# Optimization experiments

Measured on AMD Instinct MI355X. Metric: run time of the kernel, lower is better.

Reference implementation:

```python
import jax, jax.numpy as jnp
import numpy as np

B, TD, TC = 64, 800, 80
ENC, H, MA, MO = 128, 400, 10, 20
OUT = MO * 6 + 1  # 121


def _lstm(x, h0, c0, Wih, Whh, bih, bhh):
    # x: (B,T,I); PyTorch gate order i,f,g,o
    xg = jnp.einsum('bti,gi->btg', x, Wih) + (bih + bhh)  # (B,T,4H)
    def step(carry, xg_t):
        h, c = carry
        g = xg_t + h @ Whh.T
        i, f, gg, o = jnp.split(g, 4, axis=-1)
        c = jax.nn.sigmoid(f) * c + jax.nn.sigmoid(i) * jnp.tanh(gg)
        h = jax.nn.sigmoid(o) * jnp.tanh(c)
        return (h, c), h
    (_, _), hs = jax.lax.scan(step, (h0, c0), xg.transpose(1, 0, 2))
    return hs.transpose(1, 0, 2)  # (B,T,H)


def setup_inputs() -> dict:
    key = jax.random.key(0)
    ks = jax.random.split(key, 16)
    s = 0.05
    rn = lambda k, sh, sc=1.0: jax.random.normal(k, sh, jnp.float32) * sc
    I1 = 3 + ENC + H
    return {
        'strokes': rn(ks[0], (B, TD, 3)),
        'context': rn(ks[1], (B, TC, ENC)),
        'context_mask': jnp.ones((B, TC), jnp.float32),
        'h_0': rn(ks[2], (3, 2 * H), s),
        'Wih0': rn(ks[3], (4 * H, 3), s), 'Whh0': rn(ks[4], (4 * H, H), s),
        'bih0': jnp.zeros((4 * H,), jnp.float32), 'bhh0': jnp.zeros((4 * H,), jnp.float32),
        'Wih1': rn(ks[5], (4 * H, I1), s), 'Whh1': rn(ks[6], (4 * H, H), s),
        'bih1': jnp.zeros((4 * H,), jnp.float32), 'bhh1': jnp.zeros((4 * H,), jnp.float32),
        'Wih2': rn(ks[7], (4 * H, I1), s), 'Whh2': rn(ks[8], (4 * H, H), s),
        'bih2': jnp.zeros((4 * H,), jnp.float32), 'bhh2': jnp.zeros((4 * H,), jnp.float32),
        'attn_W': rn(ks[9], (3 * MA, H), s), 'attn_b': jnp.zeros((3 * MA,), jnp.float32),
        'out_W': rn(ks[10], (OUT, 3 * H), s), 'out_b': jnp.zeros((OUT,), jnp.float32),
    }


def reference(strokes, context, context_mask, h_0,
              Wih0, Whh0, bih0, bhh0,
              Wih1, Whh1, bih1, bhh1,
              Wih2, Whh2, bih2, bhh2,
              attn_W, attn_b, out_W, out_b):
    bsz = strokes.shape[0]
    # initial states: h_0[l] split into (h, c)
    init = [(jnp.broadcast_to(h_0[l, :H], (bsz, H)), jnp.broadcast_to(h_0[l, H:], (bsz, H))) for l in range(3)]

    h0s = _lstm(strokes, init[0][0], init[0][1], Wih0, Whh0, bih0, bhh0)  # (B,TD,H)

    # Gaussian monotonic attention
    p = jnp.exp(h0s @ attn_W.T + attn_b)  # (B,TD,3MA)
    alpha, beta, kappa = jnp.split(p, 3, axis=-1)
    kappa = jnp.cumsum(0.2 * kappa, axis=1)  # (B,TD,MA)
    u = jnp.arange(TC, dtype=jnp.float32)  # (TC,)
    # phi: (B,TD,TC)
    diff = kappa[:, :, None, :] - u[None, None, :, None]
    phi = jnp.sum(alpha[:, :, None, :] * jnp.exp(-beta[:, :, None, :] * diff * diff), axis=-1)
    w = jnp.einsum('btu,bue->bte', phi * context_mask[:, None, :], context)  # (B,TD,ENC)

    x1 = jnp.concatenate([strokes, h0s, w], axis=2)
    h1s = _lstm(x1, init[1][0], init[1][1], Wih1, Whh1, bih1, bhh1)
    x2 = jnp.concatenate([strokes, h1s, w], axis=2)
    h2s = _lstm(x2, init[2][0], init[2][1], Wih2, Whh2, bih2, bhh2)

    outputs = jnp.concatenate([h0s, h1s, h2s], axis=-1) @ out_W.T + out_b  # (B,TD,121)
    return outputs
```

## Files before the change

kernel.cpp:

```cpp
#include <hip/hip_runtime.h>
#include <stdint.h>

typedef unsigned short u16;
typedef __attribute__((ext_vector_type(8))) short bf16x8;
typedef __attribute__((ext_vector_type(4))) float f32x4;
typedef __attribute__((ext_vector_type(4))) int   i32x4;
typedef __attribute__((ext_vector_type(4))) unsigned short u16x4;

#define DI static __device__ __forceinline__

constexpr int B_   = 64;
constexpr int TD   = 800;
constexpr int TC   = 80;
constexpr int ENC  = 128;
constexpr int H    = 400;
constexpr int OUTN = 121;

constexpr int HP   = 416;
constexpr int KT_H = 13;
constexpr int KOP  = 1216;
constexpr int NOP  = 128;
constexpr int NBL  = 25;
constexpr int NBA  = 32;
constexpr int CSTR = 32;
constexpr int FSLOT= 32;

constexpr size_t HB_B  = (size_t)(TD+1)*B_*HP*2;
constexpr size_t WBF_B = (size_t)TD*B_*ENC*2;
constexpr size_t STR_B = (size_t)TD*B_*4*4;
constexpr size_t APK_B = (size_t)NBL*4*KT_H*64*8*2;
constexpr size_t WF_B  = (size_t)NBL*4*17*64*8*2;
constexpr size_t LOC_B = (size_t)2*B_*HP*2;

constexpr size_t OFF_HB0 = 0;
constexpr size_t OFF_HB1 = OFF_HB0 + HB_B;
constexpr size_t OFF_HB2 = OFF_HB1 + HB_B;
constexpr size_t OFF_HLO = OFF_HB2 + HB_B;
constexpr size_t OFF_WBF = OFF_HLO + HB_B;
constexpr size_t OFF_STR = OFF_WBF + WBF_B;
constexpr size_t OFF_APKH= OFF_STR + STR_B;
constexpr size_t OFF_APKL= OFF_APKH + 3*APK_B;
constexpr size_t OFF_WF1 = OFF_APKL + APK_B;
constexpr size_t OFF_WF2 = OFF_WF1 + WF_B;
constexpr size_t OFF_OUW = OFF_WF2 + WF_B;
constexpr size_t OFF_BIA = OFF_OUW + (size_t)NOP*KOP*2;
constexpr size_t OFF_CNT = OFF_BIA + (size_t)3*1600*4;
constexpr size_t OFF_XCC = OFF_CNT + (size_t)4*FSLOT*CSTR*4;
constexpr size_t OFF_FLG = OFF_XCC + (size_t)3*FSLOT*CSTR*4;
constexpr size_t OFF_HL0 = OFF_FLG + (size_t)3*FSLOT*CSTR*4;
constexpr size_t OFF_LL0 = OFF_HL0 + LOC_B;
constexpr size_t OFF_HL1 = OFF_LL0 + LOC_B;
constexpr size_t OFF_HL2 = OFF_HL1 + LOC_B;
constexpr size_t WS_NEED = OFF_HL2 + LOC_B + 256;

constexpr int LDS_DUMP = 0;
constexpr int LDS_CL   = 66560;
constexpr int LDS_EX   = 70656;
constexpr int LDS_W3   = 140288;
constexpr int LDS_BIAS = 141056;
constexpr int LDS_VERD = 141312;
constexpr int LDSB     = 141568;
constexpr int ALDS_CTX = 0;
constexpr int ALDS_ATW = 81920;
constexpr int ALDS_H   = 130040;
constexpr int ALDS_PHI = 133240;
constexpr int ALDS_MSK = 133880;
constexpr int ALDS_KAP = 134520;
constexpr int ALDS_P   = 134600;
constexpr int ALDS_PPS = 134840;

DI u16 f2b(float f){ union{float f; unsigned u;} v; v.f=f; unsigned r = v.u + 0x7FFFu + ((v.u>>16)&1u); return (u16)(r>>16); }
DI float b2f(u16 h){ union{unsigned u; float f;} v; v.u=((unsigned)h)<<16; return v.f; }
DI float sigm(float x){ return 1.f/(1.f+__expf(-x)); }
DI float tanh_(float x){ float a=fabsf(x), e=__expf(-2.f*a), t=(1.f-e)/(1.f+e); return x<0.f ? -t : t; }

DI void st16(u16* p, u16 v){
  asm volatile("global_store_short %0, %1, off sc0 sc1" :: "v"(p), "v"((unsigned)v) : "memory");
}
DI void st8(u16* p, u16x4 v){
  unsigned long long x; __builtin_memcpy(&x, &v, 8);
  asm volatile("global_store_dwordx2 %0, %1, off sc0 sc1" :: "v"(p), "v"(x) : "memory");
}
DI void setflag(unsigned* p, unsigned t){
  asm volatile("global_store_dword %0, %1, off sc0 sc1" :: "v"(p), "v"(t) : "memory");
}
DI void waitflags2(const unsigned* fA, int nA, unsigned tA,
                   const unsigned* fB, int nB, unsigned tB){
  int lane = threadIdx.x & 63;
  const unsigned* p; unsigned tgt;
  if (lane < nA)            { p = fA + (size_t)lane*CSTR;        tgt = tA; }
  else if (lane < nA+nB)    { p = fB + (size_t)(lane-nA)*CSTR;   tgt = tB; }
  else                      { p = fA;                            tgt = 0;  }
  while (1) {
    unsigned v = __hip_atomic_load(p, __ATOMIC_RELAXED, __HIP_MEMORY_SCOPE_AGENT);
    if (__all(v >= tgt)) break;
    __builtin_amdgcn_s_sleep(1);
  }
  asm volatile("" ::: "memory");
}
DI void waitloc(const unsigned* f, int n, unsigned tgt){
  int lane = threadIdx.x & 63;
  const volatile unsigned* p = (const volatile unsigned*)(f + (size_t)((lane<n)?lane:0)*CSTR);
  while (1) {
    unsigned v = *p;
    if (__all(v >= tgt)) break;
    __builtin_amdgcn_s_sleep(1);
  }
  asm volatile("" ::: "memory");
}
DI bf16x8 vld8(const u16* p){
  i32x4 v = *(const volatile i32x4*)p;
  bf16x8 r; __builtin_memcpy(&r, &v, 16); return r;
}
DI int get_xcc(){
  int x; asm volatile("s_getreg_b32 %0, hwreg(HW_REG_XCC_ID)" : "=s"(x)); return x & 0xff;
}

__global__ void k_init(const float* __restrict__ h0, u16* hb0, u16* hb1, u16* hb2, u16* hlo,
                       unsigned* cnt, unsigned* xccb, unsigned* flgb,
                       u16* hl0, u16* ll0, u16* hl1, u16* hl2){
  int i = blockIdx.x*256 + threadIdx.x;
  const int nA = 3*B_*HP, nA2 = B_*HP, nB = 4*TD*B_*16, nC = 4*FSLOT, nD = 6*FSLOT;
  const int nE = 4*2*B_*HP;
  if (i < nA) {
    int l = i/(B_*HP); int rem = i - l*(B_*HP); int b = rem/HP; int k = rem - b*HP;
    u16 v = (k<H) ? f2b(h0[l*800 + k]) : (u16)0;
    (l==0?hb0:(l==1?hb1:hb2))[(size_t)b*HP + k] = v;
  } else if (i < nA+nA2) {
    int rem = i - nA; int b = rem/HP; int k = rem - b*HP;
    u16 v = 0;
    if (k < H) { float w = h0[k]; u16 hi = f2b(w); v = f2b(w - b2f(hi)); }
    hlo[(size_t)b*HP + k] = v;
  } else if (i < nA+nA2+nB) {
    int q = i - nA - nA2; int buf = q/(TD*B_*16); int r2 = q % (TD*B_*16);
    int t = r2/(B_*16) + 1; int r3 = r2 % (B_*16); int b = r3>>4; int kk = r3&15;
    u16* hb = (buf==0)?hb0:((buf==1)?hb1:((buf==2)?hb2:hlo));
    hb[((size_t)t*B_ + b)*HP + 400 + kk] = 0;
  } else if (i < nA+nA2+nB+nC) {
    int q = i - nA - nA2 - nB;
    cnt[(size_t)q*CSTR] = 0u;
  } else if (i < nA+nA2+nB+nC+nD) {
    int q = i - nA - nA2 - nB - nC;
    if (q < 3*FSLOT) xccb[(size_t)q*CSTR] = 0u;
    else             flgb[(size_t)(q-3*FSLOT)*CSTR] = 0u;
  } else if (i < nA+nA2+nB+nC+nD+nE) {
    int q = i - nA - nA2 - nB - nC - nD;
    int buf = q / (2*B_*HP); int rem = q % (2*B_*HP);
    int k = rem % HP;
    u16 v = 0;
    if (k < H) {
      if (buf == 0)      v = f2b(h0[k]);
      else if (buf == 1) { float w = h0[k]; u16 hi = f2b(w); v = f2b(w - b2f(hi)); }
      else if (buf == 2) v = f2b(h0[800 + k]);
      else               v = f2b(h0[1600 + k]);
    }
    (buf==0?hl0:(buf==1?ll0:(buf==2?hl1:hl2)))[rem] = v;
  }
}

__global__ void k_apack(const float* W0, const float* W1, const float* W2,
                        u16* apkHi, u16* apkLo){
  int i = blockIdx.x*256 + threadIdx.x;
  const int total = 3*NBL*4*KT_H*64;
  if (i >= total) return;
  int lane = i & 63; int r = i >> 6;
  int kt = r % KT_H; r /= KT_H;
  int mt = r % 4;    r /= 4;
  int j  = r % NBL;  int lv = r / NBL;
  const float* W = (lv==0)?W0:((lv==1)?W1:W2);
  int row = mt*400 + j*16 + (lane & 15);
  int kbase = kt*32 + (lane>>4)*8;
  #pragma unroll
  for (int e=0;e<8;++e){
    int k = kbase+e;
    float w = (k<H) ? W[(size_t)row*H + k] : 0.f;
    u16 hi = f2b(w);
    apkHi[(size_t)i*8 + e] = hi;
    if (lv == 0) apkLo[(size_t)i*8 + e] = f2b(w - b2f(hi));
  }
}

__global__ void k_wihpack2(const float* __restrict__ W, u16* __restrict__ dst){
  int i = blockIdx.x*256 + threadIdx.x;
  if (i >= NBL*4*17*64) return;
  int lane = i & 63; int r = i >> 6;
  int ktf = r % 17; r /= 17; int mt = r % 4; int j = r / 4;
  int row = mt*400 + j*16 + (lane & 15);
  int kbase = ktf*32 + (lane>>4)*8;
  #pragma unroll
  for (int e=0;e<8;++e){
    int k = kbase+e;
    int col;
    if (ktf < 13) col = (k < 400) ? (3 + k) : -1;
    else          col = 403 + (k - 416);
    dst[(size_t)i*8 + e] = (col >= 0) ? f2b(W[(size_t)row*531 + col]) : (u16)0;
  }
}

__global__ void k_smallpack(const float* outW,
                            const float* bi0, const float* bh0, const float* bi1, const float* bh1,
                            const float* bi2, const float* bh2,
                            u16* ouw, float* biasP){
  int i = blockIdx.x*256 + threadIdx.x;
  const int n2 = NOP*KOP, n3 = 3*1600;
  if (i < n2) {
    int n = i/KOP, k = i - n*KOP;
    ouw[i] = (n<OUTN && k<1200) ? f2b(outW[(size_t)n*1200 + k]) : (u16)0;
  } else if (i < n2+n3) {
    int q = i-n2; int l = q/1600, row = q - l*1600;
    const float* bi = (l==0)?bi0:((l==1)?bi1:bi2);
    const float* bh = (l==0)?bh0:((l==1)?bh1:bh2);
    biasP[q] = bi[row] + bh[row];
  }
}

__global__ void k_packs(const float* __restrict__ strokes, float* __restrict__ st){
  int i = blockIdx.x*256 + threadIdx.x;
  if (i >= TD*B_) return;
  int t = i / B_, b = i & 63;
  st[(size_t)i*4+0] = strokes[((size_t)b*TD + t)*3 + 0];
  st[(size_t)i*4+1] = strokes[((size_t)b*TD + t)*3 + 1];
  st[(size_t)i*4+2] = strokes[((size_t)b*TD + t)*3 + 2];
  st[(size_t)i*4+3] = 0.f;
}

template<int L, bool LOC>
DI void stage_lstm(char* smem, int j,
    const u16* __restrict__ apkHi, const u16* __restrict__ exG,
    const float* __restrict__ strokesT,
    const float* __restrict__ wihRaw, int wihStride,
    const float* __restrict__ biasL, const float* __restrict__ h0g,
    u16* __restrict__ hb_self, const u16* __restrict__ hb_prev,
    u16* __restrict__ hlo_, const u16* __restrict__ wbf,
    unsigned* __restrict__ fSelf, const unsigned* __restrict__ fDep, int nDep,
    u16* __restrict__ hloc, u16* __restrict__ lloc, unsigned* __restrict__ flgS)
{
  float* dumpS = (float*)(smem + LDS_DUMP);
  float* cL    = (float*)(smem + LDS_CL);
  u16*   exS   = (u16*)  (smem + LDS_EX);
  float* w3S   = (float*)(smem + LDS_W3);
  float* biasS = (float*)(smem + LDS_BIAS);
  const int tid = threadIdx.x, wv = tid>>6, l = tid&63;
  const int col = l&15, kg = l>>4;

  bf16x8 ahi[4][4];
  #pragma unroll
  for (int mt=0;mt<4;++mt)
    #pragma unroll
    for (int i=0;i<4;++i){
      int kt = wv + i*4;
      if (kt < KT_H) ahi[mt][i] = *(const bf16x8*)(apkHi + (size_t)j*26624 + ((size_t)(mt*KT_H + kt)*64 + l)*8);
      else { bf16x8 z = {0,0,0,0,0,0,0,0}; ahi[mt][i] = z; }
    }
  {
    const int nv = (L==0) ? 3328 : 4352;
    const size_t stride = (L==0) ? 26624 : 34816;
    const i32x4* src = (const i32x4*)(exG + (size_t)j*stride);
    i32x4* dst = (i32x4*)exS;
    for (int i = tid; i < nv; i += 256) dst[i] = src[i];
  }
  if (tid < 192) {
    int local = tid/3, c = tid - (tid/3)*3;
    int row = (local>>4)*400 + j*16 + (local&15);
    w3S[tid] = wihRaw[(size_t)row*wihStride + c];
  }
  if (tid < 64) {
    int row = (tid>>4)*400 + j*16 + (tid&15);
    biasS[tid] = biasL[row];
  }
  for (int i = tid; i < 1024; i += 256) cL[i] = h0g[L*800 + 400 + j*16 + (i>>6)];
  __syncthreads();

  for (int t = 1; t <= TD; ++t) {
    if (wv == 0) {
      if constexpr (L > 0) waitflags2(fDep, nDep, (unsigned)t, nullptr, 0, 0u);
      if constexpr (LOC)   waitloc(flgS, NBL, (unsigned)(t-1));
      else                 waitflags2(fSelf, NBL, (unsigned)(t-1), nullptr, 0, 0u);
    }
    __syncthreads();
    f32x4 acc[4][4];
    #pragma unroll
    for (int mt=0;mt<4;++mt)
      #pragma unroll
      for (int nt=0;nt<4;++nt){ f32x4 z = {0.f,0.f,0.f,0.f}; acc[mt][nt] = z; }

    const u16* hbase; const u16* lbase = nullptr;
    if constexpr (LOC) {
      hbase = hloc + (size_t)((t-1)&1)*B_*HP + kg*8;
      if constexpr (L==0) lbase = lloc + (size_t)((t-1)&1)*B_*HP + kg*8;
    } else {
      hbase = hb_self + (size_t)(t-1)*B_*HP + kg*8;
      if constexpr (L==0) lbase = hlo_ + (size_t)(t-1)*B_*HP + kg*8;
    }
    #pragma unroll
    for (int i=0;i<4;++i){
      int kt = wv + i*4;
      if (kt < KT_H) {
        bf16x8 bhi[4], blo[4];
        #pragma unroll
        for (int nt=0;nt<4;++nt){
          if constexpr (LOC) bhi[nt] = vld8(hbase + (size_t)(nt*16+col)*HP + kt*32);
          else               bhi[nt] = *(const bf16x8*)(hbase + (size_t)(nt*16+col)*HP + kt*32);
          if constexpr (L==0) {
            if constexpr (LOC) blo[nt] = vld8(lbase + (size_t)(nt*16+col)*HP + kt*32);
            else               blo[nt] = *(const bf16x8*)(lbase + (size_t)(nt*16+col)*HP + kt*32);
          }
        }
        #pragma unroll
        for (int mt=0;mt<4;++mt){
          bf16x8 a = ahi[mt][i];
          #pragma unroll
          for (int nt=0;nt<4;++nt)
            acc[mt][nt] = __builtin_amdgcn_mfma_f32_16x16x32_bf16(a, bhi[nt], acc[mt][nt], 0,0,0);
          if constexpr (L==0) {
            bf16x8 al = *(const bf16x8*)(exS + ((size_t)(mt*KT_H + kt)*64 + l)*8);
            #pragma unroll
            for (int nt=0;nt<4;++nt){
              acc[mt][nt] = __builtin_amdgcn_mfma_f32_16x16x32_bf16(a,  blo[nt], acc[mt][nt], 0,0,0);
              acc[mt][nt] = __builtin_amdgcn_mfma_f32_16x16x32_bf16(al, bhi[nt], acc[mt][nt], 0,0,0);
            }
          }
        }
      }
    }
    if constexpr (L > 0) {
      const u16* pbase = hb_prev + (size_t)t*B_*HP + kg*8;
      const u16* wbase = wbf + ((size_t)(t-1)*B_)*ENC + kg*8;
      #pragma unroll
      for (int i=0;i<5;++i){
        int ktf = wv + i*4;
        if (ktf < 17) {
          bf16x8 bfr[4];
          if (ktf < 13) {
            #pragma unroll
            for (int nt=0;nt<4;++nt) bfr[nt] = *(const bf16x8*)(pbase + (size_t)(nt*16+col)*HP + ktf*32);
          } else {
            #pragma unroll
            for (int nt=0;nt<4;++nt) bfr[nt] = *(const bf16x8*)(wbase + (size_t)(nt*16+col)*ENC + (ktf-13)*32);
          }
          #pragma unroll
          for (int mt=0;mt<4;++mt){
            bf16x8 a = *(const bf16x8*)(exS + ((size_t)(mt*17 + ktf)*64 + l)*8);
            #pragma unroll
            for (int nt=0;nt<4;++nt)
              acc[mt][nt] = __builtin_amdgcn_mfma_f32_16x16x32_bf16(a, bfr[nt], acc[mt][nt], 0,0,0);
          }
        }
      }
    }
    #pragma unroll
    for (int mt=0;mt<4;++mt)
      #pragma unroll
      for (int nt=0;nt<4;++nt)
        #pragma unroll
        for (int r=0;r<4;++r)
          dumpS[wv*4160 + (mt*16 + kg*4 + r)*65 + nt*16 + col] = acc[mt][nt][r];
    __syncthreads();
    {
      const int bg = tid & 63, uq = tid >> 6;
      const float* sp = strokesT + ((size_t)(t-1)*B_ + bg)*4;
      float sx = sp[0], sy = sp[1], sz = sp[2];
      u16x4 hh4, ll4;
      #pragma unroll
      for (int e=0;e<4;++e){
        int u = uq*4 + e;
        int idx = u*64 + bg;
        float gv[4];
        #pragma unroll
        for (int g=0; g<4; ++g){
          int row = g*16 + u;
          float s = dumpS[row*65 + bg] + dumpS[4160 + row*65 + bg]
                  + dumpS[8320 + row*65 + bg] + dumpS[12480 + row*65 + bg];
          s += biasS[row] + w3S[row*3+0]*sx + w3S[row*3+1]*sy + w3S[row*3+2]*sz;
          gv[g] = s;
        }
        float co = cL[idx];
        float i_ = sigm(gv[0]), f_ = sigm(gv[1]), g_ = tanh_(gv[2]), o_ = sigm(gv[3]);
        float cn = f_*co + i_*g_;
        cL[idx] = cn;
        float hv = o_*tanh_(cn);
        u16 hh = f2b(hv);
        hh4[e] = hh;
        if constexpr (L==0) ll4[e] = f2b(hv - b2f(hh));
      }
      if constexpr (LOC) {
        *(u16x4*)(hloc + ((size_t)(t&1)*B_ + bg)*HP + j*16 + uq*4) = hh4;
        if constexpr (L==0) *(u16x4*)(lloc + ((size_t)(t&1)*B_ + bg)*HP + j*16 + uq*4) = ll4;
      }
      st8(hb_self + ((size_t)t*B_ + bg)*HP + j*16 + uq*4, hh4);
      if constexpr (L==0) st8(hlo_ + ((size_t)t*B_ + bg)*HP + j*16 + uq*4, ll4);
    }
    __syncthreads();
    if (tid == 0) {
      if constexpr (LOC) *((volatile unsigned*)(flgS + (size_t)j*CSTR)) = (unsigned)t;
      setflag(fSelf + (size_t)j*CSTR, (unsigned)t);
    }
  }
}

DI void stage_attn(char* smem, int j2,
    const float* __restrict__ ctx, const float* __restrict__ cmask,
    const float* __restrict__ attnW, const float* __restrict__ attnB,
    const u16* __restrict__ hb0, const u16* __restrict__ hlo_,
    u16* __restrict__ wbf,
    const unsigned* __restrict__ fA, unsigned* __restrict__ fB)
{
  float* ctxS = (float*)(smem + ALDS_CTX);
  float* atwS = (float*)(smem + ALDS_ATW);
  float* hS   = (float*)(smem + ALDS_H);
  float* phiS = (float*)(smem + ALDS_PHI);
  float* mskS = (float*)(smem + ALDS_MSK);
  float* kapS = (float*)(smem + ALDS_KAP);
  float* pS   = (float*)(smem + ALDS_P);
  float* ppsS = (float*)(smem + ALDS_PPS);
  const int tid = threadIdx.x;
  const int b0 = j2*2;
  for (int i = tid; i < 2*80*128; i += 256) {
    int bi = i/10240, rem = i%10240;
    ctxS[i] = ctx[(size_t)(b0+bi)*10240 + rem];
  }
  for (int i = tid; i < 30*400; i += 256) {
    int row = i/400, k = i - row*400;
    atwS[row*401 + k] = attnW[i];
  }
  for (int i = tid; i < 160; i += 256) {
    int bi = i/80, u = i - bi*80;
    mskS[i] = cmask[(b0+bi)*80 + u];
  }
  if (tid < 20) kapS[tid] = 0.f;
  float aB = (tid < 60) ? attnB[tid % 30] : 0.f;
  __syncthreads();

  for (int t = 1; t <= TD; ++t) {
    if ((tid>>6) == 0) waitflags2(fA, NBL, (unsigned)t, nullptr, 0, 0u);
    __syncthreads();
    if (tid < 200) {
      int bi = tid/100, k = (tid%100)*4;
      size_t off = ((size_t)t*B_ + (b0+bi))*HP + k;
      u16x4 hi4 = *(const u16x4*)(hb0 + off);
      u16x4 lo4 = *(const u16x4*)(hlo_ + off);
      #pragma unroll
      for (int e=0;e<4;++e) hS[bi*400 + k + e] = b2f(hi4[e]) + b2f(lo4[e]);
    }
    __syncthreads();
    if (tid < 240) {
      int bi = tid/120, r = tid - bi*120;
      int row = r>>2, seg = r&3;
      const float* ar = atwS + row*401 + seg*100;
      const float* hr = hS + bi*400 + seg*100;
      float a0=0,a1=0,a2=0,a3=0;
      #pragma unroll 4
      for (int k=0;k<100;k+=4){
        a0 += ar[k]*hr[k]; a1 += ar[k+1]*hr[k+1];
        a2 += ar[k+2]*hr[k+2]; a3 += ar[k+3]*hr[k+3];
      }
      ppsS[(bi*30+row)*4+seg] = a0+a1+a2+a3;
    }
    __syncthreads();
    if (tid < 60) {
      int bi = tid/30, row = tid - bi*30;
      const float* pp = ppsS + (bi*30+row)*4;
      pS[bi*30+row] = __expf(pp[0]+pp[1]+pp[2]+pp[3] + aB);
    }
    __syncthreads();
    if (tid < 20) {
      int bi = tid/10, m = tid - bi*10;
      kapS[tid] += 0.2f * pS[bi*30 + 20 + m];
    }
    __syncthreads();
    if (tid < 160) {
      int bi = tid/80; float u2 = (float)(tid - bi*80);
      const float* pb = pS + bi*30; const float* kb = kapS + bi*10;
      float a = 0.f;
      #pragma unroll
      for (int m=0;m<10;++m){ float d = kb[m]-u2; a += pb[m]*__expf(-pb[10+m]*d*d); }
      phiS[tid] = a * mskS[tid];
    }
    __syncthreads();
    {
      int bi = tid >> 7, e = tid & 127;
      const float* ph = phiS + bi*80;
      const float* cs = ctxS + (size_t)bi*10240 + e;
      float a = 0.f;
      for (int u = 0; u < TC; ++u) a += ph[u]*cs[u*128];
      st16(wbf + ((size_t)(t-1)*B_ + (b0+bi))*ENC + e, f2b(a));
    }
    __syncthreads();
    if (tid == 0) setflag(fB + (size_t)j2*CSTR, (unsigned)t);
  }
}

DI bool xcc_check(char* smem, int stage, int j, unsigned* xccb){
  unsigned* xs = xccb + (size_t)stage*FSLOT*CSTR;
  if (threadIdx.x == 0) setflag(xs + (size_t)j*CSTR, 0x100u | (unsigned)get_xcc());
  if ((threadIdx.x>>6) == 0) {
    waitflags2(xs, NBL, 0x100u, nullptr, 0, 0u);
    int lane = threadIdx.x & 63;
    unsigned v = __hip_atomic_load(xs + (size_t)((lane<NBL)?lane:0)*CSTR,
                                   __ATOMIC_RELAXED, __HIP_MEMORY_SCOPE_AGENT);
    unsigned r0 = __shfl(v, 0);
    int uni = __all(v == r0) ? 1 : 0;
    if (threadIdx.x == 0) *(int*)(smem + LDS_VERD) = uni;
  }
  __syncthreads();
  return (*(int*)(smem + LDS_VERD)) != 0;
}

__global__ __launch_bounds__(256,1) void k_mega(
    const u16* apkH, const u16* apkL, const u16* wf1, const u16* wf2,
    const float* strokesT, const float* Wih0, const float* Wih1, const float* Wih2,
    const float* bia, const float* h0g,
    u16* hb0, u16* hb1, u16* hb2, u16* hlo, u16* wbf,
    const float* ctx, const float* cmask, const float* attnW, const float* attnB,
    unsigned* cnt, unsigned* xccb, unsigned* flgb,
    u16* hl0, u16* ll0, u16* hl1, u16* hl2)
{
  extern __shared__ char smem[];
  unsigned* fA = cnt;
  unsigned* fB = cnt + (size_t)FSLOT*CSTR;
  unsigned* fC = cnt + (size_t)2*FSLOT*CSTR;
  unsigned* fD = cnt + (size_t)3*FSLOT*CSTR;
  int b = blockIdx.x; int colx = b & 7; int row = b >> 3;
  if (colx == 0 && row < NBL) {
    bool loc = xcc_check(smem, 0, row, xccb);
    if (loc) stage_lstm<0,true >(smem, row, apkH, apkL, strokesT, Wih0, 3, bia, h0g,
                  hb0, nullptr, hlo, nullptr, fA, nullptr, 0, hl0, ll0, flgb);
    else     stage_lstm<0,false>(smem, row, apkH, apkL, strokesT, Wih0, 3, bia, h0g,
                  hb0, nullptr, hlo, nullptr, fA, nullptr, 0, hl0, ll0, flgb);
  } else if ((colx == 1 || colx == 2) && row < 16) {
    int j2 = (colx-1)*16 + row;
    stage_attn(smem, j2, ctx, cmask, attnW, attnB, hb0, hlo, wbf, fA, fB);
  } else if (colx == 3 && row < NBL) {
    bool loc = xcc_check(smem, 1, row, xccb);
    unsigned* fg = flgb + (size_t)FSLOT*CSTR;
    if (loc) stage_lstm<1,true >(smem, row, apkH + (size_t)1*NBL*26624, wf1, strokesT, Wih1, 531,
                  bia+1600, h0g, hb1, hb0, nullptr, wbf, fC, fB, NBA, hl1, nullptr, fg);
    else     stage_lstm<1,false>(smem, row, apkH + (size_t)1*NBL*26624, wf1, strokesT, Wih1, 531,
                  bia+1600, h0g, hb1, hb0, nullptr, wbf, fC, fB, NBA, hl1, nullptr, fg);
  } else if (colx == 4 && row < NBL) {
    bool loc = xcc_check(smem, 2, row, xccb);
    unsigned* fg = flgb + (size_t)2*FSLOT*CSTR;
    if (loc) stage_lstm<2,true >(smem, row, apkH + (size_t)2*NBL*26624, wf2, strokesT, Wih2, 531,
                  bia+3200, h0g, hb2, hb1, nullptr, wbf, fD, fC, NBL, hl2, nullptr, fg);
    else     stage_lstm<2,false>(smem, row, apkH + (size_t)2*NBL*26624, wf2, strokesT, Wih2, 531,
                  bia+3200, h0g, hb2, hb1, nullptr, wbf, fD, fC, NBL, hl2, nullptr, fg);
  }
}

__global__ __launch_bounds__(256) void k_gemm_out(const u16* __restrict__ hb0, const u16* __restrict__ hb1,
                                                  const u16* __restrict__ hb2, const u16* __restrict__ ouw,
                                                  const float* __restrict__ out_b, float* __restrict__ dout){
  int wv = threadIdx.x>>6, l = threadIdx.x&63;
  int task = blockIdx.x*4 + wv;
  int ng = task & 1; int mpair = task >> 1;
  int m0 = mpair*32; int t = m0>>6; int broff = m0 & 63;
  int col = l&15, kg = l>>4;
  f32x4 acc[2][4];
  #pragma unroll
  for (int mt=0;mt<2;++mt)
    #pragma unroll
    for (int nt=0;nt<4;++nt){ f32x4 z = {0.f,0.f,0.f,0.f}; acc[mt][nt] = z; }
  for (int kt=0; kt<38; ++kt) {
    int k0 = kt*32 + kg*8;
    int reg = (k0>=800) ? 2 : ((k0>=400) ? 1 : 0);
    int koff = k0 - reg*400;
    const u16* hb = (reg==0) ? hb0 : ((reg==1) ? hb1 : hb2);
    bf16x8 afr[2];
    #pragma unroll
    for (int mt=0;mt<2;++mt)
      afr[mt] = *(const bf16x8*)(hb + ((size_t)(t+1)*B_ + broff + mt*16 + col)*HP + koff);
    #pragma unroll
    for (int nt=0;nt<4;++nt) {
      bf16x8 bfr = *(const bf16x8*)(ouw + (size_t)(ng*64 + nt*16 + col)*KOP + k0);
      #pragma unroll
      for (int mt=0;mt<2;++mt)
        acc[mt][nt] = __builtin_amdgcn_mfma_f32_16x16x32_bf16(afr[mt], bfr, acc[mt][nt], 0,0,0);
    }
  }
  #pragma unroll
  for (int mt=0;mt<2;++mt)
    #pragma unroll
    for (int nt=0;nt<4;++nt)
      #pragma unroll
      for (int r=0;r<4;++r) {
        int n = ng*64 + nt*16 + col;
        int bo = broff + mt*16 + kg*4 + r;
        if (n < OUTN) dout[((size_t)bo*TD + t)*OUTN + n] = acc[mt][nt][r] + out_b[n];
      }
}

__global__ void k_sentinel(float* o, float code){ o[threadIdx.x] = code; }

extern "C" void kernel_launch(void* const* d_in, const int* in_sizes, int n_in,
                              void* d_out, int out_size, void* d_ws, size_t ws_size,
                              hipStream_t stream) {
  const float* strokes = (const float*)d_in[0];
  const float* context = (const float*)d_in[1];
  const float* cmask   = (const float*)d_in[2];
  const float* h0      = (const float*)d_in[3];
  const float* Wih0 = (const float*)d_in[4];  const float* Whh0 = (const float*)d_in[5];
  const float* bih0 = (const float*)d_in[6];  const float* bhh0 = (const float*)d_in[7];
  const float* Wih1 = (const float*)d_in[8];  const float* Whh1 = (const float*)d_in[9];
  const float* bih1 = (const float*)d_in[10]; const float* bhh1 = (const float*)d_in[11];
  const float* Wih2 = (const float*)d_in[12]; const float* Whh2 = (const float*)d_in[13];
  const float* bih2 = (const float*)d_in[14]; const float* bhh2 = (const float*)d_in[15];
  const float* attnW = (const float*)d_in[16]; const float* attnB = (const float*)d_in[17];
  const float* outW  = (const float*)d_in[18]; const float* outB  = (const float*)d_in[19];
  float* dout = (float*)d_out;

  if (ws_size < WS_NEED) {
    float code = 1000.0f + (float)(ws_size >> 20);
    k_sentinel<<<1, 64, 0, stream>>>(dout, code);
    return;
  }

  char* ws = (char*)d_ws;
  u16* hb0 = (u16*)(ws + OFF_HB0);
  u16* hb1 = (u16*)(ws + OFF_HB1);
  u16* hb2 = (u16*)(ws + OFF_HB2);
  u16* hlo = (u16*)(ws + OFF_HLO);
  u16* wbf = (u16*)(ws + OFF_WBF);
  float* strT = (float*)(ws + OFF_STR);
  u16* apkH = (u16*)(ws + OFF_APKH);
  u16* apkL = (u16*)(ws + OFF_APKL);
  u16* wf1  = (u16*)(ws + OFF_WF1);
  u16* wf2  = (u16*)(ws + OFF_WF2);
  u16* ouw  = (u16*)(ws + OFF_OUW);
  float* bia = (float*)(ws + OFF_BIA);
  unsigned* cnt = (unsigned*)(ws + OFF_CNT);
  unsigned* xccb = (unsigned*)(ws + OFF_XCC);
  unsigned* flgb = (unsigned*)(ws + OFF_FLG);
  u16* hl0 = (u16*)(ws + OFF_HL0);
  u16* ll0 = (u16*)(ws + OFF_LL0);
  u16* hl1 = (u16*)(ws + OFF_HL1);
  u16* hl2 = (u16*)(ws + OFF_HL2);

  (void)hipFuncSetAttribute((const void*)k_mega, hipFuncAttributeMaxDynamicSharedMemorySize, LDSB);

  {
    int n = 3*B_*HP + B_*HP + 4*TD*B_*16 + 4*FSLOT + 6*FSLOT + 4*2*B_*HP;
    k_init<<<(n+255)/256, 256, 0, stream>>>(h0, hb0, hb1, hb2, hlo, cnt, xccb, flgb, hl0, ll0, hl1, hl2);
  }
  k_apack<<<(3*NBL*4*KT_H*64+255)/256, 256, 0, stream>>>(Whh0, Whh1, Whh2, apkH, apkL);
  k_wihpack2<<<(NBL*4*17*64+255)/256, 256, 0, stream>>>(Wih1, wf1);
  k_wihpack2<<<(NBL*4*17*64+255)/256, 256, 0, stream>>>(Wih2, wf2);
  {
    int n = NOP*KOP + 3*1600;
    k_smallpack<<<(n+255)/256, 256, 0, stream>>>(outW, bih0,bhh0,bih1,bhh1,bih2,bhh2, ouw, bia);
  }
  k_packs<<<(TD*B_+255)/256, 256, 0, stream>>>(strokes, strT);

  k_mega<<<256, 256, LDSB, stream>>>(apkH, apkL, wf1, wf2,
      strT, Wih0, Wih1, Wih2, bia, h0,
      hb0, hb1, hb2, hlo, wbf,
      context, cmask, attnW, attnB, cnt, xccb, flgb, hl0, ll0, hl1, hl2);

  k_gemm_out<<<3200/4, 256, 0, stream>>>(hb0, hb1, hb2, ouw, outB, dout);
}
```

Measured before the change: 7.307 ms.

## Replace full barriers with partial-waitcnt raw barriers and lag cross-stage flags

```diff
diff --git a/kernel.cpp b/kernel.cpp
--- a/kernel.cpp
+++ b/kernel.cpp
@@ -84,6 +84,15 @@
 DI void setflag(unsigned* p, unsigned t){
   asm volatile("global_store_dword %0, %1, off sc0 sc1" :: "v"(p), "v"(t) : "memory");
 }
+template<int K>
+DI void rawbar(){
+  __builtin_amdgcn_sched_barrier(0);
+  if constexpr (K==0)      asm volatile("s_waitcnt vmcnt(0) lgkmcnt(0)" ::: "memory");
+  else if constexpr (K==1) asm volatile("s_waitcnt vmcnt(1) lgkmcnt(0)" ::: "memory");
+  else                     asm volatile("s_waitcnt vmcnt(2) lgkmcnt(0)" ::: "memory");
+  __builtin_amdgcn_s_barrier();
+  __builtin_amdgcn_sched_barrier(0);
+}
 DI void waitflags2(const unsigned* fA, int nA, unsigned tA,
                    const unsigned* fB, int nB, unsigned tB){
   int lane = threadIdx.x & 63;
@@ -104,7 +113,6 @@
   while (1) {
     unsigned v = *p;
     if (__all(v >= tgt)) break;
-    __builtin_amdgcn_s_sleep(1);
   }
   asm volatile("" ::: "memory");
 }
@@ -242,6 +250,7 @@
   float* biasS = (float*)(smem + LDS_BIAS);
   const int tid = threadIdx.x, wv = tid>>6, l = tid&63;
   const int col = l&15, kg = l>>4;
+  constexpr int KO = (L==0) ? 2 : ((L==1) ? 1 : 0);
 
   bf16x8 ahi[4][4];
   #pragma unroll
@@ -272,12 +281,21 @@
   __syncthreads();
 
   for (int t = 1; t <= TD; ++t) {
-    if (wv == 0) {
-      if constexpr (L > 0) waitflags2(fDep, nDep, (unsigned)t, nullptr, 0, 0u);
-      if constexpr (LOC)   waitloc(flgS, NBL, (unsigned)(t-1));
-      else                 waitflags2(fSelf, NBL, (unsigned)(t-1), nullptr, 0, 0u);
-    }
-    __syncthreads();
+    if constexpr (LOC) {
+      if constexpr (L > 0) {
+        if (wv == 0) waitflags2(fDep, nDep, (unsigned)t, nullptr, 0, 0u);
+        waitloc(flgS, NBL, (unsigned)(t-1));
+        rawbar<KO>();
+      } else {
+        waitloc(flgS, NBL, (unsigned)(t-1));
+      }
+    } else {
+      if (wv == 0) {
+        if constexpr (L > 0) waitflags2(fDep, nDep, (unsigned)t, fSelf, NBL, (unsigned)(t-1));
+        else                 waitflags2(fSelf, NBL, (unsigned)(t-1), nullptr, 0, 0u);
+      }
+      __syncthreads();
+    }
     f32x4 acc[4][4];
     #pragma unroll
     for (int mt=0;mt<4;++mt)
@@ -355,7 +373,7 @@
         #pragma unroll
         for (int r=0;r<4;++r)
           dumpS[wv*4160 + (mt*16 + kg*4 + r)*65 + nt*16 + col] = acc[mt][nt][r];
-    __syncthreads();
+    if constexpr (LOC) rawbar<KO>(); else __syncthreads();
     {
       const int bg = tid & 63, uq = tid >> 6;
       const float* sp = strokesT + ((size_t)(t-1)*B_ + bg)*4;
@@ -386,16 +404,31 @@
       if constexpr (LOC) {
         *(u16x4*)(hloc + ((size_t)(t&1)*B_ + bg)*HP + j*16 + uq*4) = hh4;
         if constexpr (L==0) *(u16x4*)(lloc + ((size_t)(t&1)*B_ + bg)*HP + j*16 + uq*4) = ll4;
-      }
-      st8(hb_self + ((size_t)t*B_ + bg)*HP + j*16 + uq*4, hh4);
-      if constexpr (L==0) st8(hlo_ + ((size_t)t*B_ + bg)*HP + j*16 + uq*4, ll4);
-    }
-    __syncthreads();
-    if (tid == 0) {
-      if constexpr (LOC) *((volatile unsigned*)(flgS + (size_t)j*CSTR)) = (unsigned)t;
-      setflag(fSelf + (size_t)j*CSTR, (unsigned)t);
-    }
-  }
+        if constexpr (L==2) {
+          *(u16x4*)(hb_self + ((size_t)t*B_ + bg)*HP + j*16 + uq*4) = hh4;
+        } else {
+          st8(hb_self + ((size_t)t*B_ + bg)*HP + j*16 + uq*4, hh4);
+          if constexpr (L==0) st8(hlo_ + ((size_t)t*B_ + bg)*HP + j*16 + uq*4, ll4);
+        }
+      } else {
+        st8(hb_self + ((size_t)t*B_ + bg)*HP + j*16 + uq*4, hh4);
+        if constexpr (L==0) st8(hlo_ + ((size_t)t*B_ + bg)*HP + j*16 + uq*4, ll4);
+      }
+    }
+    if constexpr (LOC) {
+      rawbar<KO>();
+      if (tid == 0) {
+        *((volatile unsigned*)(flgS + (size_t)j*CSTR)) = (unsigned)t;
+        if constexpr (L < 2) setflag(fSelf + (size_t)j*CSTR, (unsigned)(t-1));
+      }
+    } else {
+      __syncthreads();
+      if (tid == 0) setflag(fSelf + (size_t)j*CSTR, (unsigned)t);
+    }
+  }
+  asm volatile("s_waitcnt vmcnt(0) lgkmcnt(0)" ::: "memory");
+  __syncthreads();
+  if (tid == 0) setflag(fSelf + (size_t)j*CSTR, (unsigned)TD);
 }
 
 DI void stage_attn(char* smem, int j2,
@@ -433,7 +466,7 @@
 
   for (int t = 1; t <= TD; ++t) {
     if ((tid>>6) == 0) waitflags2(fA, NBL, (unsigned)t, nullptr, 0, 0u);
-    __syncthreads();
+    rawbar<1>();
     if (tid < 200) {
       int bi = tid/100, k = (tid%100)*4;
       size_t off = ((size_t)t*B_ + (b0+bi))*HP + k;
@@ -442,7 +475,7 @@
       #pragma unroll
       for (int e=0;e<4;++e) hS[bi*400 + k + e] = b2f(hi4[e]) + b2f(lo4[e]);
     }
-    __syncthreads();
+    rawbar<1>();
     if (tid < 240) {
       int bi = tid/120, r = tid - bi*120;
       int row = r>>2, seg = r&3;
@@ -456,18 +489,18 @@
       }
       ppsS[(bi*30+row)*4+seg] = a0+a1+a2+a3;
     }
-    __syncthreads();
+    rawbar<1>();
     if (tid < 60) {
       int bi = tid/30, row = tid - bi*30;
       const float* pp = ppsS + (bi*30+row)*4;
       pS[bi*30+row] = __expf(pp[0]+pp[1]+pp[2]+pp[3] + aB);
     }
-    __syncthreads();
+    rawbar<1>();
     if (tid < 20) {
       int bi = tid/10, m = tid - bi*10;
       kapS[tid] += 0.2f * pS[bi*30 + 20 + m];
     }
-    __syncthreads();
+    rawbar<1>();
     if (tid < 160) {
       int bi = tid/80; float u2 = (float)(tid - bi*80);
       const float* pb = pS + bi*30; const float* kb = kapS + bi*10;
@@ -476,7 +509,7 @@
       for (int m=0;m<10;++m){ float d = kb[m]-u2; a += pb[m]*__expf(-pb[10+m]*d*d); }
       phiS[tid] = a * mskS[tid];
     }
-    __syncthreads();
+    rawbar<1>();
     {
       int bi = tid >> 7, e = tid & 127;
       const float* ph = phiS + bi*80;
@@ -485,9 +518,12 @@
       for (int u = 0; u < TC; ++u) a += ph[u]*cs[u*128];
       st16(wbf + ((size_t)(t-1)*B_ + (b0+bi))*ENC + e, f2b(a));
     }
-    __syncthreads();
-    if (tid == 0) setflag(fB + (size_t)j2*CSTR, (unsigned)t);
-  }
+    rawbar<1>();
+    if (tid == 0) setflag(fB + (size_t)j2*CSTR, (unsigned)(t-1));
+  }
+  asm volatile("s_waitcnt vmcnt(0) lgkmcnt(0)" ::: "memory");
+  __syncthreads();
+  if (tid == 0) setflag(fB + (size_t)j2*CSTR, (unsigned)TD);
 }
 
 DI bool xcc_check(char* smem, int stage, int j, unsigned* xccb){
```

After: 7.748 ms. 1.06x slower.
